# Kernel optimization log

Hardware: AMD Instinct MI355X
Metric: run time of the kernel (lower is better)

The kernel has to match this reference:

```python
import jax, jax.numpy as jnp
import numpy as np

T, N = 256, 128
STATE_D, TARGET_D = 64, 64
HID = 512
A, P = 8, 8
AP = A * P
REPEAT = 2
THR = 1.0  # snntorch default threshold


@jax.custom_vjp
def spike(x):
    # Heaviside with ATan surrogate gradient (snntorch default, alpha=2)
    return (x > 0.0).astype(x.dtype)

def _spike_fwd(x):
    return (x > 0.0).astype(x.dtype), x

def _spike_bwd(x, g):
    return (g / (1.0 + (jnp.pi * x) ** 2),)

spike.defvjp(_spike_fwd, _spike_bwd)


def setup_inputs() -> dict:
    key = jax.random.key(0)
    ks = jax.random.split(key, 16)
    in_dim = STATE_D + TARGET_D
    g = lambda k, shape, fan: (jax.random.uniform(k, shape, jnp.float32) * 2.0 - 1.0) / np.sqrt(fan)
    return {
        "state": jax.random.normal(ks[0], (T, N, STATE_D), jnp.float32),
        "target": jax.random.normal(ks[1], (T, N, TARGET_D), jnp.float32),
        "W_rec_in": g(ks[2], (HID, in_dim), in_dim),
        "b_rec_in": jnp.zeros((HID,), jnp.float32),
        "W_rec": g(ks[3], (HID, HID), HID),
        "b_rec": jnp.zeros((HID,), jnp.float32),
        "alpha_rec": jax.random.uniform(ks[4], (HID,), jnp.float32),
        "beta_rec": jax.random.uniform(ks[5], (HID,), jnp.float32),
        "W_ff_in": g(ks[6], (HID, HID), HID),
        "b_ff_in": jnp.zeros((HID,), jnp.float32),
        "alpha_ff": jax.random.uniform(ks[7], (HID,), jnp.float32),
        "beta_ff": jax.random.uniform(ks[8], (HID,), jnp.float32),
        "W_mu_in": g(ks[9], (AP, HID), HID),
        "b_mu_in": jnp.zeros((AP,), jnp.float32),
        "beta_mu": jax.random.uniform(ks[10], (AP,), jnp.float32),
        "W_mu_out": jnp.full((A, AP), 1.0 / P, jnp.float32),
        "W_lv_in": g(ks[11], (AP, HID), HID),
        "b_lv_in": jnp.zeros((AP,), jnp.float32),
        "beta_lv": jax.random.uniform(ks[12], (AP,), jnp.float32),
        "W_lv_out": jnp.full((A, AP), 1.0 / P, jnp.float32),
    }


def _forward(state, target, W_rec_in, b_rec_in, W_rec, b_rec, alpha_rec, beta_rec,
             W_ff_in, b_ff_in, alpha_ff, beta_ff,
             W_mu_in, b_mu_in, beta_mu, W_mu_out,
             W_lv_in, b_lv_in, beta_lv, W_lv_out):
    x_all = jnp.concatenate([state, target], axis=-1)  # [T, N, in_dim]

    def neuron_step(carry, x):
        spk_r, syn_r, mem_r, syn_f, mem_f, mem_mu, mem_lv = carry
        # --- RSynaptic (recurrent LIF with synaptic current), reset=subtract ---
        cur_r = x @ W_rec_in.T + b_rec_in + spk_r @ W_rec.T + b_rec
        reset_r = jax.lax.stop_gradient((mem_r > THR).astype(x.dtype))
        syn_r = alpha_rec * syn_r + cur_r
        mem_r = beta_rec * mem_r + syn_r - reset_r * THR
        spk_r = spike(mem_r - THR)
        # --- Synaptic feed-forward layer, reset=subtract ---
        cur_f = spk_r @ W_ff_in.T + b_ff_in
        reset_f = jax.lax.stop_gradient((mem_f > THR).astype(x.dtype))
        syn_f = alpha_ff * syn_f + cur_f
        mem_f = beta_ff * mem_f + syn_f - reset_f * THR
        spk_f = spike(mem_f - THR)
        # --- readout Synaptic neurons: alpha=0 (syn == input), reset='none' ---
        mem_mu = beta_mu * mem_mu + (spk_f @ W_mu_in.T + b_mu_in)
        mem_lv = beta_lv * mem_lv + (spk_f @ W_lv_in.T + b_lv_in)
        mu = mem_mu @ W_mu_out.T   # [N, A]
        lv = mem_lv @ W_lv_out.T   # [N, A]
        return (spk_r, syn_r, mem_r, syn_f, mem_f, mem_mu, mem_lv), (mu, lv)

    def t_step(carry, x):
        mus, lvs = [], []
        for _ in range(REPEAT):  # repeat_input, fixed and small
            carry, (mu, lv) = neuron_step(carry, x)
            mus.append(mu)
            lvs.append(lv)
        return carry, (jnp.mean(jnp.stack(mus), 0), jnp.mean(jnp.stack(lvs), 0))

    z = jnp.zeros((N, HID), state.dtype)
    z2 = jnp.zeros((N, AP), state.dtype)
    carry0 = (z, z, z, z, z, z2, z2)
    _, (mu_outs, lv_outs) = jax.lax.scan(t_step, carry0, x_all)
    return mu_outs, lv_outs  # each [T, N, A]


def reference(state, target, W_rec_in, b_rec_in, W_rec, b_rec, alpha_rec, beta_rec,
              W_ff_in, b_ff_in, alpha_ff, beta_ff,
              W_mu_in, b_mu_in, beta_mu, W_mu_out,
              W_lv_in, b_lv_in, beta_lv, W_lv_out):
    return _forward(state, target, W_rec_in, b_rec_in, W_rec, b_rec, alpha_rec, beta_rec,
                    W_ff_in, b_ff_in, alpha_ff, beta_ff,
                    W_mu_in, b_mu_in, beta_mu, W_mu_out,
                    W_lv_in, b_lv_in, beta_lv, W_lv_out)
```

## Files before the change

kernel.cpp:

```cpp
#include <hip/hip_runtime.h>


typedef unsigned int       u32;
typedef unsigned short     u16;
typedef unsigned long long u64;
typedef unsigned char      u8;

#define TSTEPS 512
#define HIDDEN 512

#define XW_OFF    0ull
#define C3_OFF    0ull
#define MEM_OFF   33554432ull
#define RING_OFF  67108864ull
#define HIST_OFF  68157440ull
#define SPKB_OFF  83886080ull
#define WT_OFF    109051904ull
#define WINT_OFF  109314048ull
#define WS_NEED   (134742016ull + 4096ull)

#define WSTRIDE 514

__global__ __launch_bounds__(256) void k_prepT(
    const float* __restrict__ Win,
    const float* __restrict__ Wmu, const float* __restrict__ Wlv,
    float* __restrict__ WinT, float* __restrict__ WT)
{
  const int idx = blockIdx.x * 256 + threadIdx.x;
  if (idx < 65536) {
    const int k = idx >> 9, j = idx & 511;
    WinT[idx] = Win[j * 128 + k];
  } else {
    const int i2 = idx - 65536;
    const int k = i2 >> 7, j = i2 & 127;
    WT[i2] = (j < 64) ? Wmu[j * 512 + k] : Wlv[(j - 64) * 512 + k];
  }
}

__global__ __launch_bounds__(256) void k_xw(
    const float* __restrict__ state, const float* __restrict__ target,
    const float* __restrict__ WinT, const float* __restrict__ b_in,
    float* __restrict__ XW)
{
  __shared__ float xs[16][129];
  const int tid  = threadIdx.x;
  const int row0 = blockIdx.x * 16;

  for (int e = tid; e < 2048; e += 256) {
    int r = e >> 7, k = e & 127;
    xs[r][k] = (k < 64) ? state[(row0 + r) * 64 + k]
                        : target[(row0 + r) * 64 + k - 64];
  }
  __syncthreads();

#pragma unroll
  for (int jh = 0; jh < 2; ++jh) {
    const int j = jh * 256 + tid;
    float acc[16];
#pragma unroll
    for (int r = 0; r < 16; ++r) acc[r] = 0.0f;
    for (int k = 0; k < 128; ++k) {
      const float wv = WinT[k * 512 + j];
#pragma unroll
      for (int r = 0; r < 16; ++r)
        acc[r] = __builtin_fmaf(xs[r][k], wv, acc[r]);
    }
    const float b = b_in[j];
#pragma unroll
    for (int r = 0; r < 16; ++r)
      XW[(u64)(row0 + r) * 512 + j] = __fadd_rn(acc[r], b);
  }
}

__global__ __launch_bounds__(512, 2) void k_rec(
    const float* __restrict__ XW,
    const float* __restrict__ Wrec, const float* __restrict__ Wff,
    const float* __restrict__ alpha_rec, const float* __restrict__ beta_rec,
    const float* __restrict__ b_rec,
    const float* __restrict__ b_ff, const float* __restrict__ alpha_ff,
    const float* __restrict__ beta_ff,
    u32* __restrict__ ring32, u32* __restrict__ hist32,
    u16* __restrict__ spkb16)
{
  __shared__ __align__(16) float WL[32 * WSTRIDE];
  __shared__ __align__(16) u16 MB[2][16][32];
  __shared__ float padlds[3584];

  const int tid  = threadIdx.x;
  const int w    = tid >> 6;
  const int l    = tid & 63;
  const bool isFF = (blockIdx.x >= 128);
  const int bb   = blockIdx.x & 127;
  const int rg   = bb >> 4;
  const int c    = bb & 15;
  const int u    = l & 31;
  const int rp   = l >> 5;
  const int rl   = 2 * w + rp;
  const int g    = 16 * rg + rl;
  const int jj   = 32 * c + u;
  const int widx = l & 31;

  {
    const float* Wsrc = isFF ? Wff : Wrec;
    for (int it = tid; it < 8192; it += 512) {
      const int uu = it >> 8, m2 = (it & 255) * 2;
      *(float2*)(WL + uu * WSTRIDE + m2) =
          *(const float2*)(Wsrc + (u64)(32 * c + uu) * 512 + m2);
    }
  }

  const float coA = isFF ? alpha_ff[jj] : alpha_rec[jj];
  const float coB = isFF ? beta_ff[jj]  : beta_rec[jj];
  const float coC = isFF ? b_ff[jj]     : b_rec[jj];

  ((volatile float*)padlds)[tid] = coC;

  const float* WLrow = WL + u * WSTRIDE;

  float syn = 0.f, mem = 0.f, spk = 0.f, xw = 0.f;

  __syncthreads();

#pragma unroll 1
  for (int s = 0; s < TSTEPS; ++s) {
    const bool doMac = isFF || (s > 0);
    const int p = isFF ? (s & 1) : ((s - 1) & 1);

    if (doMac) {
      u32 v;
      if (!isFF) {
        const u32 expct = (u32)s;
        const u32* src = ring32 + p * 4096 + g * 32 + widx;
        v = __hip_atomic_load(src, __ATOMIC_RELAXED, __HIP_MEMORY_SCOPE_AGENT);
        while ((v >> 16) != expct) {
          __builtin_amdgcn_s_sleep(1);
          v = __hip_atomic_load(src, __ATOMIC_RELAXED, __HIP_MEMORY_SCOPE_AGENT);
        }
      } else {
        const u32 expct = (u32)(s + 1);
        const u32* src = hist32 + (u64)s * 4096 + g * 32 + widx;
        v = __hip_atomic_load(src, __ATOMIC_RELAXED, __HIP_MEMORY_SCOPE_AGENT);
        while ((v >> 16) != expct) {
          __builtin_amdgcn_s_sleep(1);
          v = __hip_atomic_load(src, __ATOMIC_RELAXED, __HIP_MEMORY_SCOPE_AGENT);
        }
      }
      MB[p][rl][widx] = (u16)v;
    }

    if (!isFF && !(s & 1))
      xw = XW[((u64)(s >> 1) * 128 + g) * 512 + jj];

    float SA = 0.f;
    if (doMac) {
      const uint4* bq = (const uint4*)&MB[p][rl][0];
      const uint4 q0 = bq[0], q1 = bq[1], q2 = bq[2], q3 = bq[3];
      const u32 bw[16] = { q0.x, q0.y, q0.z, q0.w, q1.x, q1.y, q1.z, q1.w,
                           q2.x, q2.y, q2.z, q2.w, q3.x, q3.y, q3.z, q3.w };
      float aA = 0.f, aB = 0.f;
#pragma unroll
      for (int d = 0; d < 12; ++d) {
        const int word = (int)bw[d];
#pragma unroll
        for (int k4 = 0; k4 < 32; k4 += 4) {
          const float2 wa = *(const float2*)(WLrow + d * 32 + k4);
          const float2 wb = *(const float2*)(WLrow + d * 32 + k4 + 2);
          aA = __fadd_rn(aA, __int_as_float(
              __builtin_amdgcn_sbfe(word, k4 + 0, 1) & __float_as_int(wa.x)));
          aA = __fadd_rn(aA, __int_as_float(
              __builtin_amdgcn_sbfe(word, k4 + 1, 1) & __float_as_int(wa.y)));
          aA = __fadd_rn(aA, __int_as_float(
              __builtin_amdgcn_sbfe(word, k4 + 2, 1) & __float_as_int(wb.x)));
          aA = __fadd_rn(aA, __int_as_float(
              __builtin_amdgcn_sbfe(word, k4 + 3, 1) & __float_as_int(wb.y)));
        }
      }
#pragma unroll
      for (int d = 12; d < 16; ++d) {
        const int word = (int)bw[d];
#pragma unroll
        for (int k4 = 0; k4 < 32; k4 += 4) {
          const float2 wa = *(const float2*)(WLrow + d * 32 + k4);
          const float2 wb = *(const float2*)(WLrow + d * 32 + k4 + 2);
          aB = __fadd_rn(aB, __int_as_float(
              __builtin_amdgcn_sbfe(word, k4 + 0, 1) & __float_as_int(wa.x)));
          aB = __fadd_rn(aB, __int_as_float(
              __builtin_amdgcn_sbfe(word, k4 + 1, 1) & __float_as_int(wa.y)));
          aB = __fadd_rn(aB, __int_as_float(
              __builtin_amdgcn_sbfe(word, k4 + 2, 1) & __float_as_int(wb.x)));
          aB = __fadd_rn(aB, __int_as_float(
              __builtin_amdgcn_sbfe(word, k4 + 3, 1) & __float_as_int(wb.y)));
        }
      }
      SA = __fadd_rn(aA, aB);
    }

    const float cur = isFF ? __fadd_rn(SA, coC)
                           : __fadd_rn(__fadd_rn(xw, SA), coC);
    syn = __fadd_rn(__fmul_rn(coA, syn), cur);
    mem = __fsub_rn(__fadd_rn(__fmul_rn(coB, mem), syn), spk);
    spk = (mem > 1.0f) ? 1.0f : 0.0f;

    const u64 B = __ballot(spk != 0.f);
    if (!isFF) {
      if (l < 4) {
        const u32 word = (u32)(B >> (16 * l)) & 0xFFFFu;
        const int gs = 16 * rg + 2 * w + (l >> 1);
        const int wx = 2 * c + (l & 1);
        __hip_atomic_store(ring32 + (s & 1) * 4096 + gs * 32 + wx,
                           ((u32)(s + 1) << 16) | word,
                           __ATOMIC_RELAXED, __HIP_MEMORY_SCOPE_AGENT);
      } else if (l < 8) {
        const int l2 = l - 4;
        const u32 word = (u32)(B >> (16 * l2)) & 0xFFFFu;
        const int gs = 16 * rg + 2 * w + (l2 >> 1);
        const int wx = 2 * c + (l2 & 1);
        __hip_atomic_store(hist32 + (u64)s * 4096 + gs * 32 + wx,
                           ((u32)(s + 1) << 16) | word,
                           __ATOMIC_RELAXED, __HIP_MEMORY_SCOPE_AGENT);
      }
    } else {
      if (l < 4) {
        const u32 word = (u32)(B >> (16 * l)) & 0xFFFFu;
        const int gs = 16 * rg + 2 * w + (l >> 1);
        const int wx = 2 * c + (l & 1);
        spkb16[(u64)s * 4096 + gs * 32 + wx] = (u16)word;
      }
    }
  }
}

__global__ __launch_bounds__(256) void k_c3(
    const u16* __restrict__ spkb16, const float* __restrict__ WT,
    const float* __restrict__ bmu, const float* __restrict__ blv,
    float* __restrict__ c3)
{
  __shared__ __align__(8) u16 Bc[32][36];
  const int tid   = threadIdx.x;
  const int rows0 = blockIdx.x * 32;

  {
    const int r = tid >> 3, gq = tid & 7;
    const u64 vv = *(const u64*)(spkb16 + (u64)(rows0 + r) * 32 + 4 * gq);
    *(u64*)&Bc[r][4 * gq] = vv;
  }
  __syncthreads();

  const int j  = tid & 127;
  const int rh = tid >> 7;
  const float bias = (j < 64) ? bmu[j] : blv[j - 64];

  float accA[16], accB[16];
#pragma unroll
  for (int r = 0; r < 16; ++r) { accA[r] = 0.f; accB[r] = 0.f; }

  for (int wi = 0; wi < 24; ++wi) {
    u16 wrow[16];
#pragma unroll
    for (int r = 0; r < 16; ++r) wrow[r] = Bc[rh * 16 + r][wi];
    const float* wpp = WT + (wi * 16) * 128 + j;
#pragma unroll
    for (int kk = 0; kk < 16; ++kk) {
      const float wvv = wpp[kk * 128];
#pragma unroll
      for (int r = 0; r < 16; ++r) {
        const float b = (float)((wrow[r] >> kk) & 1u);
        accA[r] = __builtin_fmaf(b, wvv, accA[r]);
      }
    }
  }
  for (int wi = 24; wi < 32; ++wi) {
    u16 wrow[16];
#pragma unroll
    for (int r = 0; r < 16; ++r) wrow[r] = Bc[rh * 16 + r][wi];
    const float* wpp = WT + (wi * 16) * 128 + j;
#pragma unroll
    for (int kk = 0; kk < 16; ++kk) {
      const float wvv = wpp[kk * 128];
#pragma unroll
      for (int r = 0; r < 16; ++r) {
        const float b = (float)((wrow[r] >> kk) & 1u);
        accB[r] = __builtin_fmaf(b, wvv, accB[r]);
      }
    }
  }

#pragma unroll
  for (int r = 0; r < 16; ++r)
    c3[(u64)(rows0 + rh * 16 + r) * 128 + j] =
        __fadd_rn(__fadd_rn(accA[r], accB[r]), bias);
}

__global__ __launch_bounds__(256) void k_scan(
    const float* __restrict__ c3,
    const float* __restrict__ beta_mu, const float* __restrict__ beta_lv,
    float* __restrict__ Mem)
{
  const int tid = blockIdx.x * 256 + threadIdx.x;
  const int n = tid >> 7, ap = tid & 127;
  const float beta = (ap < 64) ? beta_mu[ap] : beta_lv[ap - 64];
  const float* src = c3 + n * 128 + ap;
  float* dst = Mem + n * 128 + ap;
  float mem = 0.0f;
  for (int t = 0; t < 512; ++t) {
    mem = __fadd_rn(__fmul_rn(beta, mem), src[(u64)t * 16384]);
    dst[(u64)t * 16384] = mem;
  }
}

__global__ __launch_bounds__(256) void k_out(
    const float* __restrict__ Mem,
    const float* __restrict__ Wmu_out, const float* __restrict__ Wlv_out,
    float* __restrict__ out)
{
  const int tid = blockIdx.x * 256 + threadIdx.x;
  const int a = tid & 7;
  const int n = (tid >> 3) & 127;
  const int t = (tid >> 10) & 255;
  const int kind = tid >> 18;
  const float* wv = ((kind == 0) ? Wmu_out : Wlv_out) + a * 64;
  const float* s0 = Mem + ((u64)(2 * t) * 128 + n) * 128 + kind * 64;
  const float* s1 = Mem + ((u64)(2 * t + 1) * 128 + n) * 128 + kind * 64;
  float mu0 = 0.0f, mu1 = 0.0f;
#pragma unroll 8
  for (int q = 0; q < 64; ++q) mu0 = __builtin_fmaf(s0[q], wv[q], mu0);
#pragma unroll 8
  for (int q = 0; q < 64; ++q) mu1 = __builtin_fmaf(s1[q], wv[q], mu1);
  out[tid] = __fmul_rn(__fadd_rn(mu0, mu1), 0.5f);
}

extern "C" void kernel_launch(void* const* d_in, const int* in_sizes, int n_in,
                              void* d_out, int out_size, void* d_ws, size_t ws_size,
                              hipStream_t stream) {
  (void)in_sizes; (void)n_in; (void)out_size;
  if (ws_size < WS_NEED) return;

  const float* state     = (const float*)d_in[0];
  const float* target    = (const float*)d_in[1];
  const float* W_rec_in  = (const float*)d_in[2];
  const float* b_rec_in  = (const float*)d_in[3];
  const float* W_rec     = (const float*)d_in[4];
  const float* b_rec     = (const float*)d_in[5];
  const float* alpha_rec = (const float*)d_in[6];
  const float* beta_rec  = (const float*)d_in[7];
  const float* W_ff_in   = (const float*)d_in[8];
  const float* b_ff_in   = (const float*)d_in[9];
  const float* alpha_ff  = (const float*)d_in[10];
  const float* beta_ff   = (const float*)d_in[11];
  const float* W_mu_in   = (const float*)d_in[12];
  const float* b_mu_in   = (const float*)d_in[13];
  const float* beta_mu   = (const float*)d_in[14];
  const float* W_mu_out  = (const float*)d_in[15];
  const float* W_lv_in   = (const float*)d_in[16];
  const float* b_lv_in   = (const float*)d_in[17];
  const float* beta_lv   = (const float*)d_in[18];
  const float* W_lv_out  = (const float*)d_in[19];

  char* ws = (char*)d_ws;
  float* XW    = (float*)(ws + XW_OFF);
  float* c3    = (float*)(ws + C3_OFF);
  float* Mem   = (float*)(ws + MEM_OFF);
  u32*   ring32= (u32*)  (ws + RING_OFF);
  u32*   hist32= (u32*)  (ws + HIST_OFF);
  u16*   spkb16= (u16*)  (ws + SPKB_OFF);
  float* WT    = (float*)(ws + WT_OFF);
  float* WinT  = (float*)(ws + WINT_OFF);

  hipMemsetAsync(ws + RING_OFF, 0, 32768, stream);
  hipMemsetAsync(ws + HIST_OFF, 0, 8388608, stream);

  hipLaunchKernelGGL(k_prepT, dim3(512), dim3(256), 0, stream,
                     W_rec_in, W_mu_in, W_lv_in, WinT, WT);
  hipLaunchKernelGGL(k_xw, dim3(2048), dim3(256), 0, stream,
                     state, target, WinT, b_rec_in, XW);
  hipLaunchKernelGGL(k_rec, dim3(256), dim3(512), 0, stream,
                     XW, W_rec, W_ff_in,
                     alpha_rec, beta_rec, b_rec,
                     b_ff_in, alpha_ff, beta_ff, ring32, hist32, spkb16);
  hipLaunchKernelGGL(k_c3, dim3(2048), dim3(256), 0, stream,
                     spkb16, WT, b_mu_in, b_lv_in, c3);
  hipLaunchKernelGGL(k_scan, dim3(64), dim3(256), 0, stream,
                     c3, beta_mu, beta_lv, Mem);
  hipLaunchKernelGGL(k_out, dim3(2048), dim3(256), 0, stream,
                     Mem, W_mu_out, W_lv_out, (float*)d_out);
}
```

Measured before the change: 4.546 ms.

## Co-locate recurrent and feedforward waves per block and prioritize recurrent waves

Recurrent and feedforward neurons previously ran in separate blocks. Each block now holds four recurrent waves and four feedforward waves covering the same 32-column slice over 8 batch rows, with both weight slices kept in LDS. The LDS padding array and the double-buffered spike-word staging are removed in favour of per-row buffers. Recurrent waves are raised with s_setprio so the serial critical chain gets issue priority over the lagging feedforward consumer. The cost is double the weight LDS per block, which limits residency, and feedforward waves now share compute units with the latency-critical recurrent chain.

```diff
diff --git a/kernel.cpp b/kernel.cpp
--- a/kernel.cpp
+++ b/kernel.cpp
@@ -82,55 +82,55 @@
     u32* __restrict__ ring32, u32* __restrict__ hist32,
     u16* __restrict__ spkb16)
 {
-  __shared__ __align__(16) float WL[32 * WSTRIDE];
-  __shared__ __align__(16) u16 MB[2][16][32];
-  __shared__ float padlds[3584];
+  __shared__ __align__(16) float WR[32 * WSTRIDE];
+  __shared__ __align__(16) float WF[32 * WSTRIDE];
+  __shared__ __align__(16) u16 MBr[8][32];
+  __shared__ __align__(16) u16 MBf[8][32];
 
   const int tid  = threadIdx.x;
   const int w    = tid >> 6;
   const int l    = tid & 63;
-  const bool isFF = (blockIdx.x >= 128);
-  const int bb   = blockIdx.x & 127;
-  const int rg   = bb >> 4;
-  const int c    = bb & 15;
+  const bool isFF = (w >= 4);
+  const int wl   = w & 3;
+  const int rg   = blockIdx.x >> 4;
+  const int c    = blockIdx.x & 15;
   const int u    = l & 31;
   const int rp   = l >> 5;
-  const int rl   = 2 * w + rp;
-  const int g    = 16 * rg + rl;
+  const int rl   = 2 * wl + rp;
+  const int g    = 8 * rg + rl;
   const int jj   = 32 * c + u;
   const int widx = l & 31;
 
-  {
-    const float* Wsrc = isFF ? Wff : Wrec;
-    for (int it = tid; it < 8192; it += 512) {
-      const int uu = it >> 8, m2 = (it & 255) * 2;
-      *(float2*)(WL + uu * WSTRIDE + m2) =
-          *(const float2*)(Wsrc + (u64)(32 * c + uu) * 512 + m2);
-    }
+  for (int it = tid; it < 8192; it += 512) {
+    const int uu = it >> 8, m2 = (it & 255) * 2;
+    *(float2*)(WR + uu * WSTRIDE + m2) =
+        *(const float2*)(Wrec + (u64)(32 * c + uu) * 512 + m2);
+    *(float2*)(WF + uu * WSTRIDE + m2) =
+        *(const float2*)(Wff + (u64)(32 * c + uu) * 512 + m2);
   }
 
   const float coA = isFF ? alpha_ff[jj] : alpha_rec[jj];
   const float coB = isFF ? beta_ff[jj]  : beta_rec[jj];
   const float coC = isFF ? b_ff[jj]     : b_rec[jj];
 
-  ((volatile float*)padlds)[tid] = coC;
-
-  const float* WLrow = WL + u * WSTRIDE;
+  const float* WLrow = (isFF ? WF : WR) + u * WSTRIDE;
+  u16* MBrow = (isFF ? MBf : MBr)[rl];
 
   float syn = 0.f, mem = 0.f, spk = 0.f, xw = 0.f;
 
   __syncthreads();
+
+  if (!isFF) __builtin_amdgcn_s_setprio(1);
 
 #pragma unroll 1
   for (int s = 0; s < TSTEPS; ++s) {
     const bool doMac = isFF || (s > 0);
-    const int p = isFF ? (s & 1) : ((s - 1) & 1);
 
     if (doMac) {
       u32 v;
       if (!isFF) {
         const u32 expct = (u32)s;
-        const u32* src = ring32 + p * 4096 + g * 32 + widx;
+        const u32* src = ring32 + ((s - 1) & 1) * 4096 + g * 32 + widx;
         v = __hip_atomic_load(src, __ATOMIC_RELAXED, __HIP_MEMORY_SCOPE_AGENT);
         while ((v >> 16) != expct) {
           __builtin_amdgcn_s_sleep(1);
@@ -145,7 +145,7 @@
           v = __hip_atomic_load(src, __ATOMIC_RELAXED, __HIP_MEMORY_SCOPE_AGENT);
         }
       }
-      MB[p][rl][widx] = (u16)v;
+      MBrow[widx] = (u16)v;
     }
 
     if (!isFF && !(s & 1))
@@ -153,7 +153,7 @@
 
     float SA = 0.f;
     if (doMac) {
-      const uint4* bq = (const uint4*)&MB[p][rl][0];
+      const uint4* bq = (const uint4*)MBrow;
       const uint4 q0 = bq[0], q1 = bq[1], q2 = bq[2], q3 = bq[3];
       const u32 bw[16] = { q0.x, q0.y, q0.z, q0.w, q1.x, q1.y, q1.z, q1.w,
                            q2.x, q2.y, q2.z, q2.w, q3.x, q3.y, q3.z, q3.w };
@@ -202,10 +202,11 @@
     spk = (mem > 1.0f) ? 1.0f : 0.0f;
 
     const u64 B = __ballot(spk != 0.f);
+    const int rowbase = 8 * rg + 2 * wl;
     if (!isFF) {
       if (l < 4) {
         const u32 word = (u32)(B >> (16 * l)) & 0xFFFFu;
-        const int gs = 16 * rg + 2 * w + (l >> 1);
+        const int gs = rowbase + (l >> 1);
         const int wx = 2 * c + (l & 1);
         __hip_atomic_store(ring32 + (s & 1) * 4096 + gs * 32 + wx,
                            ((u32)(s + 1) << 16) | word,
@@ -213,7 +214,7 @@
       } else if (l < 8) {
         const int l2 = l - 4;
         const u32 word = (u32)(B >> (16 * l2)) & 0xFFFFu;
-        const int gs = 16 * rg + 2 * w + (l2 >> 1);
+        const int gs = rowbase + (l2 >> 1);
         const int wx = 2 * c + (l2 & 1);
         __hip_atomic_store(hist32 + (u64)s * 4096 + gs * 32 + wx,
                            ((u32)(s + 1) << 16) | word,
@@ -222,7 +223,7 @@
     } else {
       if (l < 4) {
         const u32 word = (u32)(B >> (16 * l)) & 0xFFFFu;
-        const int gs = 16 * rg + 2 * w + (l >> 1);
+        const int gs = rowbase + (l >> 1);
         const int wx = 2 * c + (l & 1);
         spkb16[(u64)s * 4096 + gs * 32 + wx] = (u16)word;
       }
```

Measured after the change: 3.927 ms. -13.6%, faster.
